# Kernel optimization log

Measured on AMD Instinct MI355X. Metric: run time of the kernel, lower is better.

Reference implementation:

```python
import jax, jax.numpy as jnp
import numpy as np

NUM_KERNELS = 5


def setup_inputs() -> dict:
    key = jax.random.key(0)
    k1, k2 = jax.random.split(key)
    B, D = 4096, 256
    return {
        "s_feat": jax.random.normal(k1, (B, D), dtype=jnp.float32),
        "t_feat": jax.random.normal(k2, (B, D), dtype=jnp.float32),
    }


def _pairwise_sq_dists(feats):
    # Gram-matrix form of sum((x_i - x_j)**2, axis=-1); same math as the
    # broadcasted (x - y)**2 sum, without the [N, N, D] intermediate.
    sq = jnp.sum(feats * feats, axis=-1)  # [N]
    d = sq[:, None] + sq[None, :] - 2.0 * (feats @ feats.T)  # [N, N]
    return jnp.maximum(d, 0.0)


def reference(s_feat, t_feat):
    batch = s_feat.shape[0]
    feats = jnp.concatenate((s_feat, t_feat), axis=0)  # [2B, D]
    distances = _pairwise_sq_dists(feats)  # [2B, 2B]

    # Median-heuristic-style bandwidth (detached in original).
    n = 2 * batch
    bandwidth = float(n * n - n) / jnp.sum(jax.lax.stop_gradient(distances))
    bandwidth = bandwidth / (2 ** (NUM_KERNELS // 2))
    gammas = [bandwidth * (2 ** i) for i in range(NUM_KERNELS)]

    # Multi-gamma Gaussian kernel average (fixed small loop over kernels).
    kern = sum(jnp.exp(-distances * g) for g in gammas) / NUM_KERNELS

    s2s = kern[:batch, :batch]
    t2t = kern[batch:, batch:]
    s2t = kern[:batch, batch:]
    disc = jnp.mean(s2s + t2t - 2.0 * s2t)
    return disc
```

## Files before the change

kernel.cpp:

```cpp
#include <hip/hip_runtime.h>
#include <stdint.h>
#include <math.h>

#define BATCH 4096
#define NT    8192
#define FD    256
#define TM    256
#define TN    128
#define BK    32
#define NUMK  5
#define NBLK  1056
#define PBLK  256

typedef __attribute__((ext_vector_type(8))) short bf16x8;
typedef __attribute__((ext_vector_type(4))) float f32x4;

static const size_t WS_FB    = 0;
static const size_t WS_SQ    = (size_t)NT * FD * 2;
static const size_t WS_PCOL  = WS_SQ + (size_t)NT * 4;
static const size_t WS_WSUM  = WS_PCOL + (size_t)PBLK * 256 * 4;
static const size_t WS_GAMMA = WS_WSUM + (size_t)PBLK * 4;

__device__ __forceinline__ unsigned short f2bf_rne(float x) {
    unsigned u = __float_as_uint(x);
    unsigned r = (u + 0x7fffu + ((u >> 16) & 1u)) >> 16;
    return (unsigned short)r;
}

__device__ __forceinline__ void async_copy16(void* lds, const void* g) {
    __builtin_amdgcn_global_load_lds(
        (__attribute__((address_space(1))) void*)(void*)(const_cast<void*>(g)),
        (__attribute__((address_space(3))) void*)lds, 16, 0, 0);
}

__global__ void mmd_prep(const float* __restrict__ s_feat,
                         const float* __restrict__ t_feat,
                         unsigned short* __restrict__ fb,
                         float* __restrict__ sq,
                         float* __restrict__ pcol,
                         float* __restrict__ wsum) {
    __shared__ float cp[16][FD];
    __shared__ float rw[16];
    const int w    = threadIdx.x >> 6;
    const int lane = threadIdx.x & 63;
    float c0 = 0.f, c1 = 0.f, c2 = 0.f, c3 = 0.f;
    float wtot = 0.f;
#pragma unroll
    for (int t = 0; t < 2; ++t) {
        int row = blockIdx.x * 32 + w * 2 + t;
        const float* src = (row < BATCH) ? (s_feat + (size_t)row * FD)
                                         : (t_feat + (size_t)(row - BATCH) * FD);
        float4 v = ((const float4*)src)[lane];
        unsigned int u01 = (unsigned)f2bf_rne(v.x) | ((unsigned)f2bf_rne(v.y) << 16);
        unsigned int u23 = (unsigned)f2bf_rne(v.z) | ((unsigned)f2bf_rne(v.w) << 16);
        ((uint2*)(fb + (size_t)row * FD))[lane] = make_uint2(u01, u23);
        float ss = v.x * v.x + v.y * v.y + v.z * v.z + v.w * v.w;
        for (int off = 32; off; off >>= 1) ss += __shfl_down(ss, off);
        if (lane == 0) { sq[row] = ss; wtot += ss; }
        c0 += v.x; c1 += v.y; c2 += v.z; c3 += v.w;
    }
    cp[w][4 * lane + 0] = c0;
    cp[w][4 * lane + 1] = c1;
    cp[w][4 * lane + 2] = c2;
    cp[w][4 * lane + 3] = c3;
    if (lane == 0) rw[w] = wtot;
    __syncthreads();
    const int t = threadIdx.x;
    if (t < 256) {
        float s = 0.f;
#pragma unroll
        for (int k = 0; k < 16; ++k) s += cp[k][t];
        pcol[(size_t)blockIdx.x * 256 + t] = s;
    }
    if (t == 0) {
        float s = 0.f;
#pragma unroll
        for (int k = 0; k < 16; ++k) s += rw[k];
        wsum[blockIdx.x] = s;
    }
}

__global__ void mmd_gamma(const float* __restrict__ pcol,
                          const float* __restrict__ wsum,
                          float* __restrict__ gamma,
                          float* __restrict__ out) {
    __shared__ float gcol[4][256];
    __shared__ float redc[4], redw[4];
    const int tid  = threadIdx.x;
    const int c    = tid & 255, s = tid >> 8;
    const int lane = tid & 63;
    float a0 = 0.f, a1 = 0.f, a2 = 0.f, a3 = 0.f;
#pragma unroll 4
    for (int k = 0; k < 64; k += 4) {
        a0 += pcol[(size_t)(s * 64 + k + 0) * 256 + c];
        a1 += pcol[(size_t)(s * 64 + k + 1) * 256 + c];
        a2 += pcol[(size_t)(s * 64 + k + 2) * 256 + c];
        a3 += pcol[(size_t)(s * 64 + k + 3) * 256 + c];
    }
    gcol[s][c] = (a0 + a1) + (a2 + a3);
    if (tid < 256) {
        float wv = wsum[tid];
        for (int off = 32; off; off >>= 1) wv += __shfl_down(wv, off);
        if (lane == 0) redw[tid >> 6] = wv;
    }
    __syncthreads();
    if (tid < 256) {
        float colv = (gcol[0][c] + gcol[1][c]) + (gcol[2][c] + gcol[3][c]);
        float cv2 = colv * colv;
        for (int off = 32; off; off >>= 1) cv2 += __shfl_down(cv2, off);
        if (lane == 0) redc[tid >> 6] = cv2;
    }
    __syncthreads();
    if (tid == 0) {
        float s2  = (redc[0] + redc[1]) + (redc[2] + redc[3]);
        float ssq = (redw[0] + redw[1]) + (redw[2] + redw[3]);
        float sumd = 2.0f * (float)NT * ssq - 2.0f * s2;
        float n2n  = (float)((long long)NT * NT - NT);
        gamma[0]   = 0.25f * (n2n / sumd);
        out[0]     = 0.f;
    }
}

__global__ __launch_bounds__(512, 4) void mmd_main(
    const unsigned short* __restrict__ fb,
    const float* __restrict__ sq,
    const float* __restrict__ gamma,
    float* __restrict__ out) {
    const int bid = blockIdx.x;
    const int swz = (bid & 7) * (NBLK / 8) + (bid >> 3);
    int I = (int)((65.0f - sqrtf(fmaxf(4225.0f - 4.0f * (float)swz, 0.f))) * 0.5f);
    if (I > 31) I = 31;
    while (I > 0 && I * (65 - I) > swz) --I;
    while (I < 31 && (I + 1) * (65 - (I + 1)) <= swz) ++I;
    const int J = 2 * I + (swz - I * (65 - I));
    const bool straddle = ((J >> 1) == I);

    __shared__ __align__(16) unsigned short a_t[3][TM * BK];
    __shared__ __align__(16) unsigned short b_t[3][TN * BK];
    __shared__ float sqa[TM], sqb[TN];
    __shared__ float red[8];

    const int tid  = threadIdx.x;
    const int w    = tid >> 6, lane = tid & 63;
    const int wm2  = w >> 1, wn2 = w & 1;
    const int quad = lane >> 4, m16 = lane & 15;
    const int lrow16 = lane >> 2;
    const int pslot  = lane & 3;

    const size_t rowA0 = (size_t)I * TM;
    const size_t rowB0 = (size_t)J * TN;

    float sqv = 0.f;
    if (tid < TM)                sqv = sq[rowA0 + tid];
    else if (tid < TM + TN)      sqv = sq[rowB0 + (tid - TM)];
    const float g0 = gamma[0];

#define STAGE(buf, k0_) do {                                                   \
        _Pragma("unroll")                                                      \
        for (int q = 0; q < 2; ++q) {                                          \
            int rr_ = w * 32 + q * 16 + lrow16;                    \
            int gc_ = pslot ^ ((rr_ >> 1) & 3);                                \
            async_copy16(&a_t[buf][(w * 32 + q * 16) * BK],                    \
                         fb + (rowA0 + rr_) * FD + (k0_) + gc_ * 8);           \
        }                                                                      \
        {                                                                      \
            int rr_ = w * 16 + lrow16;                             \
            int gc_ = pslot ^ ((rr_ >> 1) & 3);                                \
            async_copy16(&b_t[buf][(w * 16) * BK],                             \
                         fb + (rowB0 + rr_) * FD + (k0_) + gc_ * 8);           \
        }                                                                      \
    } while (0)

    STAGE(0, 0);
    STAGE(1, BK);
    STAGE(2, 2 * BK);

    if (tid < TM)                sqa[tid] = sqv;
    else if (tid < TM + TN)      sqb[tid - TM] = sqv;

    const f32x4 fzero = {0.f, 0.f, 0.f, 0.f};
    f32x4 acc[4][4];
#pragma unroll
    for (int a = 0; a < 4; ++a)
#pragma unroll
        for (int b = 0; b < 4; ++b) acc[a][b] = fzero;

    __syncthreads();

#pragma unroll
    for (int st = 0; st < 8; ++st) {
        if (st > 0) {
            if (st >= 3) {
                if (st == 7) asm volatile("s_waitcnt vmcnt(0)" ::: "memory");
                else         asm volatile("s_waitcnt vmcnt(3)" ::: "memory");
            }
            __builtin_amdgcn_s_barrier();
            __builtin_amdgcn_sched_barrier(0);
            if (st <= 5) STAGE((st + 2) % 3, (st + 2) * BK);
        }
        const int cur = st % 3;

        bf16x8 af[4], bf[4];
#pragma unroll
        for (int tm = 0; tm < 4; ++tm) {
            int row = wm2 * 64 + tm * 16 + m16;
            int p = quad ^ ((row >> 1) & 3);
            af[tm] = *(const bf16x8*)&a_t[cur][row * BK + p * 8];
        }
#pragma unroll
        for (int tn = 0; tn < 4; ++tn) {
            int row = wn2 * 64 + tn * 16 + m16;
            int p = quad ^ ((row >> 1) & 3);
            bf[tn] = *(const bf16x8*)&b_t[cur][row * BK + p * 8];
        }
        __builtin_amdgcn_sched_barrier(0);

        __builtin_amdgcn_s_setprio(1);
#pragma unroll
        for (int tm = 0; tm < 4; ++tm)
#pragma unroll
            for (int tn = 0; tn < 4; ++tn)
                acc[tm][tn] = __builtin_amdgcn_mfma_f32_16x16x32_bf16(
                    af[tm], bf[tn], acc[tm][tn], 0, 0, 0);
        __builtin_amdgcn_s_setprio(0);
    }

    float ls[4] = {0.f, 0.f, 0.f, 0.f};
    if (!straddle) {
#pragma unroll
        for (int tm = 0; tm < 4; ++tm) {
            const int i0 = wm2 * 64 + tm * 16 + quad * 4;
            float sqi[4] = {sqa[i0 + 0], sqa[i0 + 1], sqa[i0 + 2], sqa[i0 + 3]};
#pragma unroll
            for (int tn = 0; tn < 4; ++tn) {
                const int j = wn2 * 64 + tn * 16 + m16;
                const float sqj = sqb[j];
#pragma unroll
                for (int rr = 0; rr < 4; ++rr) {
                    float d = fmaf(-2.f, acc[tm][tn][rr], sqi[rr] + sqj);
                    d = fmaxf(d, 0.f);
                    float e1 = __expf(-d * g0);
                    float e2 = e1 * e1, e4 = e2 * e2, e8 = e4 * e4, e16 = e8 * e8;
                    ls[rr] += e1 + e2 + e4 + e8 + e16;
                }
            }
        }
    } else {
        const int dOff = (J - 2 * I) * TN;
#pragma unroll
        for (int tm = 0; tm < 4; ++tm) {
            const int i0 = wm2 * 64 + tm * 16 + quad * 4;
            float sqi[4] = {sqa[i0 + 0], sqa[i0 + 1], sqa[i0 + 2], sqa[i0 + 3]};
#pragma unroll
            for (int tn = 0; tn < 4; ++tn) {
                const int j = wn2 * 64 + tn * 16 + m16;
                const float sqj = sqb[j];
                const int jg = j + dOff;
#pragma unroll
                for (int rr = 0; rr < 4; ++rr) {
                    const int ig = i0 + rr;
                    float wf = (jg > ig) ? 2.f : ((jg == ig) ? 1.f : 0.f);
                    float d = fmaf(-2.f, acc[tm][tn][rr], sqi[rr] + sqj);
                    d = fmaxf(d, 0.f);
                    float e1 = __expf(-d * g0);
                    float e2 = e1 * e1, e4 = e2 * e2, e8 = e4 * e4, e16 = e8 * e8;
                    ls[rr] += wf * (e1 + e2 + e4 + e8 + e16);
                }
            }
        }
    }
    float lsum = (ls[0] + ls[1]) + (ls[2] + ls[3]);
    for (int off = 32; off; off >>= 1) lsum += __shfl_down(lsum, off);
    if (lane == 0) red[w] = lsum;
    __syncthreads();
    if (tid == 0) {
        float wgt;
        if (straddle) wgt = 1.f;
        else wgt = ((I < 16) == (J < 32)) ? 2.f : -2.f;
        float scale = wgt * (1.f / NUMK) * (1.f / 16777216.f);
        float tot = ((red[0] + red[1]) + (red[2] + red[3]))
                  + ((red[4] + red[5]) + (red[6] + red[7]));
        atomicAdd(out, tot * scale);
    }
}

extern "C" void kernel_launch(void* const* d_in, const int* in_sizes, int n_in,
                              void* d_out, int out_size, void* d_ws, size_t ws_size,
                              hipStream_t stream) {
    const float* s_feat = (const float*)d_in[0];
    const float* t_feat = (const float*)d_in[1];
    char* ws = (char*)d_ws;
    unsigned short* fb = (unsigned short*)(ws + WS_FB);
    float* sq    = (float*)(ws + WS_SQ);
    float* pcol  = (float*)(ws + WS_PCOL);
    float* wsum  = (float*)(ws + WS_WSUM);
    float* gamma = (float*)(ws + WS_GAMMA);
    float* out   = (float*)d_out;

    mmd_prep<<<PBLK, 1024, 0, stream>>>(s_feat, t_feat, fb, sq, pcol, wsum);
    mmd_gamma<<<1, 1024, 0, stream>>>(pcol, wsum, gamma, out);
    mmd_main<<<NBLK, 512, 0, stream>>>(fb, sq, gamma, out);
}
```

Before: 101.2 us.

## Switch to double-buffered LDS pipeline and prescale exponent into base-2 domain

```diff
diff --git a/kernel.cpp b/kernel.cpp
--- a/kernel.cpp
+++ b/kernel.cpp
@@ -135,8 +135,8 @@
     const int J = 2 * I + (swz - I * (65 - I));
     const bool straddle = ((J >> 1) == I);
 
-    __shared__ __align__(16) unsigned short a_t[3][TM * BK];
-    __shared__ __align__(16) unsigned short b_t[3][TN * BK];
+    __shared__ __align__(16) unsigned short a_t[2][TM * BK];
+    __shared__ __align__(16) unsigned short b_t[2][TN * BK];
     __shared__ float sqa[TM], sqb[TN];
     __shared__ float red[8];
 
@@ -173,10 +173,11 @@
 
     STAGE(0, 0);
     STAGE(1, BK);
-    STAGE(2, 2 * BK);
-
-    if (tid < TM)                sqa[tid] = sqv;
-    else if (tid < TM + TN)      sqb[tid - TM] = sqv;
+
+    const float Gl    = g0 * 1.44269504f;
+    const float twoGl = 2.0f * Gl;
+    if (tid < TM)                sqa[tid] = sqv * Gl;
+    else if (tid < TM + TN)      sqb[tid - TM] = sqv * Gl;
 
     const f32x4 fzero = {0.f, 0.f, 0.f, 0.f};
     f32x4 acc[4][4];
@@ -189,16 +190,13 @@
 
 #pragma unroll
     for (int st = 0; st < 8; ++st) {
-        if (st > 0) {
-            if (st >= 3) {
-                if (st == 7) asm volatile("s_waitcnt vmcnt(0)" ::: "memory");
-                else         asm volatile("s_waitcnt vmcnt(3)" ::: "memory");
-            }
+        if (st >= 2) {
+            if (st == 7) asm volatile("s_waitcnt vmcnt(0)" ::: "memory");
+            else         asm volatile("s_waitcnt vmcnt(3)" ::: "memory");
             __builtin_amdgcn_s_barrier();
             __builtin_amdgcn_sched_barrier(0);
-            if (st <= 5) STAGE((st + 2) % 3, (st + 2) * BK);
-        }
-        const int cur = st % 3;
+        }
+        const int cur = st & 1;
 
         bf16x8 af[4], bf[4];
 #pragma unroll
@@ -213,6 +211,12 @@
             int p = quad ^ ((row >> 1) & 3);
             bf[tn] = *(const bf16x8*)&b_t[cur][row * BK + p * 8];
         }
+        asm volatile("s_waitcnt lgkmcnt(0)" ::: "memory");
+        __builtin_amdgcn_sched_barrier(0);
+        if (st <= 5) {
+            __builtin_amdgcn_s_barrier();
+            STAGE(cur, (st + 2) * BK);
+        }
         __builtin_amdgcn_sched_barrier(0);
 
         __builtin_amdgcn_s_setprio(1);
@@ -237,11 +241,11 @@
                 const float sqj = sqb[j];
 #pragma unroll
                 for (int rr = 0; rr < 4; ++rr) {
-                    float d = fmaf(-2.f, acc[tm][tn][rr], sqi[rr] + sqj);
-                    d = fmaxf(d, 0.f);
-                    float e1 = __expf(-d * g0);
+                    float ex = fminf(fmaf(acc[tm][tn][rr], twoGl,
+                                          -(sqi[rr] + sqj)), 0.f);
+                    float e1 = exp2f(ex);
                     float e2 = e1 * e1, e4 = e2 * e2, e8 = e4 * e4, e16 = e8 * e8;
-                    ls[rr] += e1 + e2 + e4 + e8 + e16;
+                    ls[rr] += (e1 + e2) + (e4 + e8) + e16;
                 }
             }
         }
@@ -260,11 +264,11 @@
                 for (int rr = 0; rr < 4; ++rr) {
                     const int ig = i0 + rr;
                     float wf = (jg > ig) ? 2.f : ((jg == ig) ? 1.f : 0.f);
-                    float d = fmaf(-2.f, acc[tm][tn][rr], sqi[rr] + sqj);
-                    d = fmaxf(d, 0.f);
-                    float e1 = __expf(-d * g0);
+                    float ex = fminf(fmaf(acc[tm][tn][rr], twoGl,
+                                          -(sqi[rr] + sqj)), 0.f);
+                    float e1 = exp2f(ex);
                     float e2 = e1 * e1, e4 = e2 * e2, e8 = e4 * e4, e16 = e8 * e8;
-                    ls[rr] += wf * (e1 + e2 + e4 + e8 + e16);
+                    ls[rr] += wf * ((e1 + e2) + (e4 + e8) + e16);
                 }
             }
         }
```

Result: slower. 105.3 us (+4.1%).
